# Kernel optimization log

Measured on AMD Instinct MI355X. Metric: run time of the kernel, lower is better.

The kernel has to match this reference:

```python
import jax, jax.numpy as jnp
import numpy as np
from functools import partial

NUM_HEADS = 12
RATIO_ACT = 0.5   # prune_ratio_act_store
RATIO_ATTN = 0.5  # prune_ratio_attn_mat_store


def kth_mask(x, ratio):
    # torch.kthvalue semantics: threshold = k-th SMALLEST of |x| over the flat tensor
    n = x.size
    k = int(np.clip(n * ratio, 1, n))
    mag = jnp.abs(x)
    thr = jnp.sort(mag.reshape(-1))[k - 1]
    return (mag >= thr).astype(x.dtype)


def st(dense, prune):
    # straight-through: value = dense, gradient flows through `prune` path
    return jax.lax.stop_gradient(dense) + prune - jax.lax.stop_gradient(prune)


def _softmax_prune_impl(x, ratio):
    dense = jax.nn.softmax(x, axis=-1)
    mask = kth_mask(dense, ratio)
    return dense, mask * dense


@partial(jax.custom_vjp, nondiff_argnums=(1,))
def softmax_prune(x, ratio):
    return _softmax_prune_impl(x, ratio)


def _sp_fwd(x, ratio):
    dense, sparse = _softmax_prune_impl(x, ratio)
    return (dense, sparse), sparse


def _sp_bwd(ratio, A, cots):
    # custom backward uses the SPARSE probs in the softmax Jacobian; the
    # cotangent of the sparse output is ignored (matches the torch Function)
    g_dense, _ = cots
    g = A * (g_dense - jnp.sum(g_dense * A, axis=-1, keepdims=True))
    return (g,)


softmax_prune.defvjp(_sp_fwd, _sp_bwd)


def setup_inputs() -> dict:
    key = jax.random.key(0)
    ks = jax.random.split(key, 5)
    B, S, H = 8, 577, 768
    hs = jax.random.normal(ks[0], (B, S, H), dtype=jnp.float32)
    w = lambda k: jax.random.normal(k, (H, H), dtype=jnp.float32) * 0.02
    z = jnp.zeros((H,), dtype=jnp.float32)
    return {
        "hidden_states": hs,
        "Wq": w(ks[1]), "bq": z,
        "Wk": w(ks[2]), "bk": z,
        "Wv": w(ks[3]), "bv": z,
        "Wo": w(ks[4]), "bo": z,
    }


def attention_forward(hidden_states, Wq, bq, Wk, bk, Wv, bv, Wo, bo):
    B, S, H = hidden_states.shape
    nh, hd = NUM_HEADS, H // NUM_HEADS
    sg = jax.lax.stop_gradient
    lin = lambda x, W, b: x @ W + b

    # prune hidden states by global magnitude threshold
    hs_p = sg(kth_mask(hidden_states, RATIO_ACT)) * hidden_states

    q = st(lin(hidden_states, Wq, bq), lin(hs_p, Wq, bq))
    k = st(lin(hidden_states, Wk, bk), lin(hs_p, Wk, bk))
    v = st(lin(hidden_states, Wv, bv), lin(hs_p, Wv, bv))

    heads = lambda x: x.reshape(B, S, nh, hd).transpose(0, 2, 1, 3)  # [B,h,S,d]
    q, k, v = heads(q), heads(k), heads(v)

    qp = sg(kth_mask(q, RATIO_ACT)) * q
    kp = sg(kth_mask(k, RATIO_ACT)) * k

    scores = st(jnp.einsum('bhqd,bhkd->bhqk', q, k),
                jnp.einsum('bhqd,bhkd->bhqk', qp, kp))
    scores = scores / float(np.sqrt(hd))

    probs, probs_p = softmax_prune(scores, RATIO_ATTN)  # dropout rate = 0 -> identity

    vp = sg(kth_mask(v, RATIO_ACT)) * v
    ctx = st(jnp.einsum('bhqk,bhkd->bhqd', probs, v),
             jnp.einsum('bhqk,bhkd->bhqd', probs_p, vp))

    ctx = ctx.transpose(0, 2, 1, 3).reshape(B, S, H)
    ctx_p = sg(kth_mask(ctx, RATIO_ACT)) * ctx

    out = st(lin(ctx, Wo, bo), lin(ctx_p, Wo, bo))
    return out  # vis=False -> weights is None


def reference(hidden_states, Wq, bq, Wk, bk, Wv, bv, Wo, bo):
    return attention_forward(hidden_states, Wq, bq, Wk, bk, Wv, bv, Wo, bo)
```

## Files before the change

### kernel.cpp

```cpp
#include <hip/hip_runtime.h>
#include <hip/hip_bf16.h>


#define B_ 8
#define S_ 577
#define H_ 768
#define NH_ 12
#define HD_ 64
#define M_ (B_*S_)
#define MPAD 4736
#define BH_ (B_*NH_)
#define SKPAD 640
#define LTS 136

typedef __attribute__((ext_vector_type(8))) short short8;
typedef __attribute__((ext_vector_type(4))) short s16x4;
typedef __attribute__((ext_vector_type(4))) float f32x4;

__device__ inline unsigned short f2bf(float f){
    unsigned int u = __float_as_uint(f);
    u = u + 0x7fffu + ((u>>16)&1u);
    return (unsigned short)(u>>16);
}

__device__ inline void gload_lds16(const short* g, short* l){
    __builtin_amdgcn_global_load_lds((const __attribute__((address_space(1))) void*)g,
                                     (__attribute__((address_space(3))) void*)l, 16, 0, 0);
}

__global__ __launch_bounds__(256) void k_prep(
    const float* __restrict__ hs, short* __restrict__ abf,
    const float* __restrict__ Wq, const float* __restrict__ Wk,
    const float* __restrict__ Wv, const float* __restrict__ Wo,
    short* __restrict__ Tq, short* __restrict__ Tk,
    short* __restrict__ Tv, short* __restrict__ To,
    short* __restrict__ kh, short* __restrict__ vt)
{
    const int bid = blockIdx.x, t = threadIdx.x;
    if(bid < 1776){
        int i = bid*256 + t;
        if(bid >= 1731){ *(short8*)(abf + (size_t)i*8) = (short8){}; return; }
        const float4* p = (const float4*)(hs + (size_t)i*8);
        float4 a = p[0], b = p[1];
        short8 v;
        v[0]=(short)f2bf(a.x); v[1]=(short)f2bf(a.y); v[2]=(short)f2bf(a.z); v[3]=(short)f2bf(a.w);
        v[4]=(short)f2bf(b.x); v[5]=(short)f2bf(b.y); v[6]=(short)f2bf(b.z); v[7]=(short)f2bf(b.w);
        *(short8*)(abf + (size_t)i*8) = v;
    } else if(bid < 2352){
        int zidx = bid - 1776;
        int z = zidx & 3, rem = zidx >> 2;
        int kx = rem % 12, ny = rem / 12;
        const float* W = z==0?Wq: z==1?Wk: z==2?Wv:Wo;
        short*       T = z==0?Tq: z==1?Tk: z==2?Tv:To;
        __shared__ float lds[64][65];
        int k0 = kx*64, n0 = ny*64;
        for(int i=0;i<4;i++){
            int row = i*16 + (t>>4);
            int col = (t&15)*4;
            float4 v = *(const float4*)&W[(k0+row)*768 + n0 + col];
            lds[row][col]=v.x; lds[row][col+1]=v.y; lds[row][col+2]=v.z; lds[row][col+3]=v.w;
        }
        __syncthreads();
        for(int i=0;i<4;i++){
            int n = i*16 + (t>>4);
            int k4 = (t&15)*4;
            for(int j=0;j<4;j++)
                T[(n0+n)*768 + k0 + k4 + j] = (short)f2bf(lds[k4+j][n]);
        }
    } else {
        int tid = (bid-2352)*256 + t;
        short8 z = {};
        if(tid < 48384){
            int row_id = tid>>3, ch = tid&7;
            int bh = row_id/63, r = row_id - bh*63;
            *(short8*)&kh[((size_t)bh*SKPAD + 577 + r)*64 + ch*8] = z;
        } else if(tid < 97536){
            int j = tid - 48384;
            int row_id = j>>3, ch = j&7;
            int bh = row_id>>6, d = row_id&63;
            *(short8*)&vt[((size_t)bh*64 + d)*SKPAD + 576 + ch*8] = z;
        }
    }
}

__global__ __launch_bounds__(512) void k_gemm(
    const short* __restrict__ A, const short* __restrict__ T,
    const float* __restrict__ b0, const float* __restrict__ b1, const float* __restrict__ b2,
    short* __restrict__ oq, short* __restrict__ ok, short* __restrict__ ovt,
    float* __restrict__ of, int mode, int NT)
{
    __shared__ short sh[32768];
    const int t = threadIdx.x;

    const int nwg = gridDim.x;
    const int q8 = nwg>>3, r8 = nwg&7;
    const int xcd = blockIdx.x&7, cidx = blockIdx.x>>3;
    const int wg = (xcd<r8 ? xcd*(q8+1) : r8*(q8+1) + (xcd-r8)*q8) + cidx;
    const int mt = wg/NT, ntile = wg - mt*NT;
    const int m0 = mt*128, n0 = ntile*128;

    const int seg = (mode==3)? 0 : n0/768;
    const float* bias = (mode==3)? b0 : (seg==0?b0: seg==1?b1:b2);
    const int nlb = (mode==3)? n0 : n0 - seg*768;

    const int w = t>>6, lane = t&63, g = lane>>4, c = lane&15;
    const int wm = w>>1, wn = w&1;

    const int lrow = lane>>3;
    const int lcol = ((lane&7) ^ lrow) * 8;
    const short* pa = A + (size_t)(m0 + w*8 + lrow)*768 + lcol;
    const short* pb = T + (size_t)(n0 + w*8 + lrow)*768 + lcol;

    f32x4 acc[2][4] = {};

    #pragma unroll
    for(int i=0;i<2;i++){
        gload_lds16(pa + (size_t)(i*64)*768, &sh[(i*64 + w*8)*64]);
        gload_lds16(pb + (size_t)(i*64)*768, &sh[8192 + (i*64 + w*8)*64]);
    }
    int bb = 0;
    for(int kk=0; kk<12; kk++){
        if(kk<11){
            short* dstA = &sh[(bb^1)*16384];
            short* dstB = dstA + 8192;
            #pragma unroll
            for(int i=0;i<2;i++){
                gload_lds16(pa + (size_t)(i*64)*768 + (kk+1)*64, &dstA[(i*64 + w*8)*64]);
                gload_lds16(pb + (size_t)(i*64)*768 + (kk+1)*64, &dstB[(i*64 + w*8)*64]);
            }
            asm volatile("s_waitcnt vmcnt(4)" ::: "memory");
        } else {
            asm volatile("s_waitcnt vmcnt(0)" ::: "memory");
        }
        __builtin_amdgcn_s_barrier();
        asm volatile("" ::: "memory");

        const short* LA = &sh[bb*16384];
        const short* LB = LA + 8192;
        short8 af[2][2], bfv[4][2];
        #pragma unroll
        for(int mi=0; mi<2; mi++){
            int row = wm*32 + mi*16 + c;
            int rx = (row&7)<<3;
            af[mi][0] = *(const short8*)&LA[row*64 + ((g*8) ^ rx)];
            af[mi][1] = *(const short8*)&LA[row*64 + ((32 + g*8) ^ rx)];
        }
        #pragma unroll
        for(int ni=0; ni<4; ni++){
            int row = wn*64 + ni*16 + c;
            int rx = (row&7)<<3;
            bfv[ni][0] = *(const short8*)&LB[row*64 + ((g*8) ^ rx)];
            bfv[ni][1] = *(const short8*)&LB[row*64 + ((32 + g*8) ^ rx)];
        }
        __builtin_amdgcn_s_setprio(1);
        #pragma unroll
        for(int mi=0; mi<2; mi++)
            #pragma unroll
            for(int ni=0; ni<4; ni++){
                acc[mi][ni] = __builtin_amdgcn_mfma_f32_16x16x32_bf16(af[mi][0], bfv[ni][0], acc[mi][ni], 0,0,0);
                acc[mi][ni] = __builtin_amdgcn_mfma_f32_16x16x32_bf16(af[mi][1], bfv[ni][1], acc[mi][ni], 0,0,0);
            }
        __builtin_amdgcn_s_setprio(0);
        asm volatile("s_waitcnt lgkmcnt(0)" ::: "memory");
        __builtin_amdgcn_s_barrier();
        asm volatile("" ::: "memory");
        bb ^= 1;
    }

    if(mode==3){
        #pragma unroll
        for(int mi=0; mi<2; mi++) for(int ni=0; ni<4; ni++){
            #pragma unroll
            for(int r=0; r<4; r++){
                int m = m0 + wm*32 + mi*16 + g*4 + r;
                int n = n0 + wn*64 + ni*16 + c;
                if(m >= M_) continue;
                of[(size_t)m*768 + n] = acc[mi][ni][r] + bias[n];
            }
        }
        return;
    }

    if(seg==2){
        #pragma unroll
        for(int mi=0;mi<2;mi++)
            #pragma unroll
            for(int ni=0;ni<4;ni++){
                int nl_ = wn*64 + ni*16 + c;
                float bv = bias[nlb + nl_];
                s16x4 pk;
                #pragma unroll
                for(int r=0;r<4;r++) pk[r] = (short)f2bf(acc[mi][ni][r] + bv);
                int ml0 = wm*32 + mi*16 + g*4;
                *(s16x4*)&sh[nl_*LTS + ml0] = pk;
            }
    } else {
        #pragma unroll
        for(int mi=0;mi<2;mi++)
            #pragma unroll
            for(int ni=0;ni<4;ni++){
                int nl_ = wn*64 + ni*16 + c;
                float bv = bias[nlb + nl_];
                #pragma unroll
                for(int r=0;r<4;r++){
                    int ml = wm*32 + mi*16 + g*4 + r;
                    sh[ml*LTS + nl_] = (short)f2bf(acc[mi][ni][r] + bv);
                }
            }
    }
    __syncthreads();

    #pragma unroll
    for(int i=0;i<4;i++){
        int idx = i*512 + t;
        int rp = idx>>4, ch = idx&15;
        short8 v8 = *(const short8*)&sh[rp*LTS + ch*8];
        if(seg==2){
            int nl = nlb + rp, hh = nl>>6, dd = nl&63;
            int mg = m0 + ch*8;
            if(mg < M_){
                int b0_ = mg/S_, s0 = mg - b0_*S_;
                if(s0+7 < S_ && mg+7 < M_){
                    *(short8*)&ovt[(((size_t)b0_*NH_+hh)*HD_+dd)*SKPAD + s0] = v8;
                } else {
                    for(int j=0;j<8;j++){
                        int m=mg+j;
                        if(m<M_){ int bj=m/S_, sj=m-bj*S_;
                            ovt[(((size_t)bj*NH_+hh)*HD_+dd)*SKPAD+sj]=v8[j]; }
                    }
                }
            }
        } else {
            int m = m0 + rp;
            if(m < M_){
                int b0_ = m/S_, s0 = m - b0_*S_;
                int nl = nlb + ch*8, hh = nl>>6, dd = nl&63;
                if(seg==1) *(short8*)&ok[(((size_t)b0_*NH_+hh)*SKPAD + s0)*HD_ + dd] = v8;
                else       *(short8*)&oq[(((size_t)b0_*NH_+hh)*S_   + s0)*HD_ + dd] = v8;
            }
        }
    }
}

__global__ __launch_bounds__(256) void k_attn(
    const short* __restrict__ qh, const short* __restrict__ kh, const short* __restrict__ vt,
    short* __restrict__ ctx)
{
    __shared__ short lK[2][64*64], lV[2][64*64], lP[4*2048];
    const int t = threadIdx.x;
    const int w = t>>6, lane = t&63, g = lane>>4, c = lane&15;
    const int bh = blockIdx.x, b = bh/NH_, h = bh%NH_;
    const int q0 = blockIdx.y*128;

    #pragma unroll
    for(int i=0;i<4;i++){
        int row = i*8 + (lane>>3);
        int e8 = (lane&7)*8;
        int s = q0 + w*32 + row;
        short8 v = {};
        if(s < S_) v = *(const short8*)&qh[((size_t)bh*S_ + s)*HD_ + e8];
        *(short8*)&lP[w*2048 + row*64 + (e8 ^ ((row&7)<<3))] = v;
    }
    short8 qf[2][2];
    #pragma unroll
    for(int qi=0; qi<2; qi++)
        #pragma unroll
        for(int ks=0; ks<2; ks++)
            qf[qi][ks] = *(const short8*)&lP[w*2048 + (qi*16+c)*64 + ((ks*32+g*8) ^ ((c&7)<<3))];

    short8 ones;
    #pragma unroll
    for(int j=0;j<8;j++) ones[j] = (short)0x3F80;

    const int srow = lane>>3;
    const int sw8 = ((lane&7) ^ srow)*8;
    const short* pk0 = kh + ((size_t)bh*SKPAD + w*16 + srow)*64 + sw8;
    const short* pv0 = vt + ((size_t)bh*64 + w*16 + srow)*SKPAD + sw8;

    #pragma unroll
    for(int i=0;i<2;i++){
        gload_lds16(pk0 + i*8*64,    &lK[0][(w*16+i*8)*64]);
        gload_lds16(pv0 + i*8*SKPAD, &lV[0][(w*16+i*8)*64]);
    }

    float m_run[2][4], l_run[2][4];
    f32x4 O[2][4] = {};
    #pragma unroll
    for(int qi=0;qi<2;qi++)
        #pragma unroll
        for(int r=0;r<4;r++){ m_run[qi][r] = -3e38f; l_run[qi][r] = 0.f; }

    int bb = 0;
    for(int kt=0; kt<10; kt++){
        if(kt<9){
            const short* pk = pk0 + (kt+1)*4096;
            const short* pv = pv0 + (kt+1)*64;
            #pragma unroll
            for(int i=0;i<2;i++){
                gload_lds16(pk + i*8*64,    &lK[bb^1][(w*16+i*8)*64]);
                gload_lds16(pv + i*8*SKPAD, &lV[bb^1][(w*16+i*8)*64]);
            }
            asm volatile("s_waitcnt vmcnt(4)" ::: "memory");
        } else {
            asm volatile("s_waitcnt vmcnt(0)" ::: "memory");
        }
        __builtin_amdgcn_s_barrier();
        asm volatile("" ::: "memory");

        const short* LK = lK[bb]; const short* LV = lV[bb];

        float sv[2][4][4];
        #pragma unroll
        for(int nt=0; nt<4; nt++){
            int row = nt*16 + c;
            int rx = (row&7)<<3;
            short8 kf[2];
            kf[0] = *(const short8*)&LK[row*64 + ((g*8) ^ rx)];
            kf[1] = *(const short8*)&LK[row*64 + ((32+g*8) ^ rx)];
            __builtin_amdgcn_s_setprio(1);
            #pragma unroll
            for(int qi=0; qi<2; qi++){
                f32x4 sa = {};
                sa = __builtin_amdgcn_mfma_f32_16x16x32_bf16(qf[qi][0], kf[0], sa, 0,0,0);
                sa = __builtin_amdgcn_mfma_f32_16x16x32_bf16(qf[qi][1], kf[1], sa, 0,0,0);
                #pragma unroll
                for(int r=0;r<4;r++) sv[qi][nt][r] = sa[r]*0.18033688011f;
            }
            __builtin_amdgcn_s_setprio(0);
        }
        if(kt==9){
            #pragma unroll
            for(int nt=0; nt<4; nt++){
                int key = 576 + nt*16 + c;
                if(key >= S_){
                    #pragma unroll
                    for(int qi=0;qi<2;qi++)
                        #pragma unroll
                        for(int r=0;r<4;r++) sv[qi][nt][r] = -3e38f;
                }
            }
        }
        float fac[2][4];
        #pragma unroll
        for(int qi=0; qi<2; qi++)
            #pragma unroll
            for(int r=0;r<4;r++){
                float mx = fmaxf(fmaxf(sv[qi][0][r],sv[qi][1][r]),fmaxf(sv[qi][2][r],sv[qi][3][r]));
                for(int off=1; off<16; off<<=1) mx = fmaxf(mx, __shfl_xor(mx, off));
                float nm = fmaxf(m_run[qi][r], mx);
                fac[qi][r] = __builtin_amdgcn_exp2f(m_run[qi][r] - nm);
                m_run[qi][r] = nm;
            }
        #pragma unroll
        for(int qi=0; qi<2; qi++)
            #pragma unroll
            for(int nt=0; nt<4; nt++)
                #pragma unroll
                for(int r=0;r<4;r++){
                    float p = __builtin_amdgcn_exp2f(sv[qi][nt][r] - m_run[qi][r]);
                    int prow = g*4 + r;
                    lP[w*2048 + qi*1024 + prow*64 + ((nt*16 + c) ^ ((prow&7)<<3))] = (short)f2bf(p);
                }
        short8 pf[2][2];
        #pragma unroll
        for(int qi=0; qi<2; qi++)
            #pragma unroll
            for(int ks=0; ks<2; ks++)
                pf[qi][ks] = *(const short8*)&lP[w*2048 + qi*1024 + c*64 + ((ks*32+g*8) ^ ((c&7)<<3))];
        __builtin_amdgcn_s_setprio(1);
        #pragma unroll
        for(int qi=0; qi<2; qi++){
            f32x4 rs = {};
            rs = __builtin_amdgcn_mfma_f32_16x16x32_bf16(pf[qi][0], ones, rs, 0,0,0);
            rs = __builtin_amdgcn_mfma_f32_16x16x32_bf16(pf[qi][1], ones, rs, 0,0,0);
            #pragma unroll
            for(int r=0;r<4;r++) l_run[qi][r] = l_run[qi][r]*fac[qi][r] + rs[r];
        }
        __builtin_amdgcn_s_setprio(0);
        #pragma unroll
        for(int qi=0; qi<2; qi++)
            #pragma unroll
            for(int nt=0;nt<4;nt++)
                #pragma unroll
                for(int r=0;r<4;r++) O[qi][nt][r] *= fac[qi][r];

        __builtin_amdgcn_s_setprio(1);
        #pragma unroll
        for(int nt=0; nt<4; nt++){
            int vrow = nt*16 + c;
            int rx = (vrow&7)<<3;
            short8 vf[2];
            vf[0] = *(const short8*)&LV[vrow*64 + ((g*8) ^ rx)];
            vf[1] = *(const short8*)&LV[vrow*64 + ((32+g*8) ^ rx)];
            #pragma unroll
            for(int qi=0; qi<2; qi++){
                O[qi][nt] = __builtin_amdgcn_mfma_f32_16x16x32_bf16(pf[qi][0], vf[0], O[qi][nt], 0,0,0);
                O[qi][nt] = __builtin_amdgcn_mfma_f32_16x16x32_bf16(pf[qi][1], vf[1], O[qi][nt], 0,0,0);
            }
        }
        __builtin_amdgcn_s_setprio(0);
        asm volatile("s_waitcnt lgkmcnt(0)" ::: "memory");
        __builtin_amdgcn_s_barrier();
        asm volatile("" ::: "memory");
        bb ^= 1;
    }

    #pragma unroll
    for(int qi=0; qi<2; qi++)
        #pragma unroll
        for(int nt=0; nt<4; nt++)
            #pragma unroll
            for(int r=0;r<4;r++){
                int s = q0 + w*32 + qi*16 + g*4 + r;
                if(s < S_){
                    float val = O[qi][nt][r] / l_run[qi][r];
                    ctx[((size_t)b*S_ + s)*H_ + h*HD_ + nt*16 + c] = (short)f2bf(val);
                }
            }
}

extern "C" void kernel_launch(void* const* d_in, const int* in_sizes, int n_in,
                              void* d_out, int out_size, void* d_ws, size_t ws_size,
                              hipStream_t stream)
{
    const float* hs = (const float*)d_in[0];
    const float* Wq = (const float*)d_in[1];
    const float* bq = (const float*)d_in[2];
    const float* Wk = (const float*)d_in[3];
    const float* bk = (const float*)d_in[4];
    const float* Wv = (const float*)d_in[5];
    const float* bv = (const float*)d_in[6];
    const float* Wo = (const float*)d_in[7];
    const float* bo = (const float*)d_in[8];
    float* out = (float*)d_out;

    char* ws = (char*)d_ws;
    short* abf = (short*)(ws);
    short* ctx = abf;
    short* wqt = (short*)(ws + 7274496);
    short* wkt = (short*)(ws + 7274496 + 1179648);
    short* wvt = (short*)(ws + 7274496 + 2*1179648);
    short* wot = (short*)(ws + 7274496 + 3*1179648);
    short* qh  = (short*)(ws + 11993088);
    short* kh  = (short*)(ws + 19083264);
    short* vt  = (short*)(ws + 26947584);

    k_prep<<<2733, 256, 0, stream>>>(hs, abf, Wq,Wk,Wv,Wo, wqt,wkt,wvt,wot, kh, vt);
    k_gemm<<<666, 512, 0, stream>>>(abf, wqt, bq,bk,bv, qh,kh,vt, nullptr, 0, 18);
    k_attn<<<dim3(96,5), 256, 0, stream>>>(qh, kh, vt, ctx);
    k_gemm<<<222, 512, 0, stream>>>(ctx, wot, bo,bo,bo, nullptr,nullptr,nullptr, out, 3, 6);
}
```

Measured before the change: 90.36 us.

## Use dedicated 256x256-tile QKV GEMM kernel with staged double-buffered LDS

Moves the QKV projection out of the generic GEMM into a new kernel with 256x256 tiles, 128 KB of double-buffered LDS and a phased MFMA schedule that prefetches the next k-tile while computing. The epilogue is split into two passes that write the Q/K/V head layouts. Larger tiles raise operand reuse and cut the number of tile loads, but the grid drops from 666 to 171 workgroups on a 256-CU part, which leaves many CUs idle. The output-projection GEMM is simplified to a single fp32-output mode.

```diff
diff --git a/kernel.cpp b/kernel.cpp
--- a/kernel.cpp
+++ b/kernel.cpp
@@ -12,6 +12,7 @@
 #define BH_ (B_*NH_)
 #define SKPAD 640
 #define LTS 136
+#define LTS2 264
 
 typedef __attribute__((ext_vector_type(8))) short short8;
 typedef __attribute__((ext_vector_type(4))) short s16x4;
@@ -83,11 +84,223 @@
     }
 }
 
+__global__ __launch_bounds__(512) void k_qkv(
+    const short* __restrict__ A, const short* __restrict__ T,
+    const float* __restrict__ b0, const float* __restrict__ b1, const float* __restrict__ b2,
+    short* __restrict__ oq, short* __restrict__ ok, short* __restrict__ ovt)
+{
+    __shared__ short sh[65536];
+    const int t = threadIdx.x;
+
+    const int nwg = gridDim.x;
+    const int q8 = nwg>>3, r8 = nwg&7;
+    const int xcd = blockIdx.x&7, cidx = blockIdx.x>>3;
+    const int wg = (xcd<r8 ? xcd*(q8+1) : r8*(q8+1) + (xcd-r8)*q8) + cidx;
+    const int mt = wg/9, nt9 = wg - mt*9;
+    const int m0 = mt*256, n0 = nt9*256;
+    const int seg = n0/768;
+    const float* bias = (seg==0?b0: seg==1?b1:b2);
+    const int nlb = n0 - seg*768;
+
+    const int w = t>>6, lane = t&63, g = lane>>4, c = lane&15;
+    const int wm = w>>2, wn = w&3;
+
+    const int srow = t>>3, sch = t&7;
+    const int sx = (sch ^ (srow&7))*8;
+    const short* pa[2][2]; const short* pb[2][2];
+    #pragma unroll
+    for(int hf=0; hf<2; hf++)
+        #pragma unroll
+        for(int i=0;i<2;i++){
+            int rga = m0 + hf*128 + i*64 + srow;
+            if(rga > 4735) rga = 4735;
+            pa[hf][i] = A + (size_t)rga*768 + sx;
+            pb[hf][i] = T + (size_t)(n0 + hf*128 + i*64 + srow)*768 + sx;
+        }
+    const int dof = srow*64 + sch*8;
+
+    f32x4 acc[8][4] = {};
+
+    #define STAGE(tt) { int pS = ((tt)&1)*16384; int kof = (tt)*64;              \
+        _Pragma("unroll") for(int hf=0; hf<2; hf++){                             \
+            _Pragma("unroll") for(int i=0;i<2;i++){                              \
+                gload_lds16(pa[hf][i] + kof, &sh[pS + hf*8192 + i*4096 + dof]);  \
+                gload_lds16(pb[hf][i] + kof, &sh[32768 + pS + hf*8192 + i*4096 + dof]); } } }
+
+    STAGE(0);
+    asm volatile("s_waitcnt vmcnt(0)" ::: "memory");
+    __builtin_amdgcn_s_barrier();
+    asm volatile("" ::: "memory");
+
+    for(int kt=0; kt<12; kt++){
+        const int p = (kt&1)*16384;
+        const short* LA = &sh[p + wm*8192];
+        const short* LB = &sh[32768 + p + (wn>>1)*8192];
+        const int brow0 = (wn&1)*64;
+
+        short8 af[4][2], af2[4][2], bfv[4][2];
+        #pragma unroll
+        for(int mi=0; mi<4; mi++){
+            int rih = mi*16 + c, rx = (rih&7)<<3;
+            af[mi][0] = *(const short8*)&LA[rih*64 + ((g*8) ^ rx)];
+            af[mi][1] = *(const short8*)&LA[rih*64 + ((32+g*8) ^ rx)];
+        }
+        #pragma unroll
+        for(int ni=0; ni<2; ni++){
+            int rih = brow0 + ni*16 + c, rx = (rih&7)<<3;
+            bfv[ni][0] = *(const short8*)&LB[rih*64 + ((g*8) ^ rx)];
+            bfv[ni][1] = *(const short8*)&LB[rih*64 + ((32+g*8) ^ rx)];
+        }
+        if(kt < 11) STAGE(kt+1);
+        __builtin_amdgcn_s_barrier();
+        asm volatile("s_waitcnt lgkmcnt(0)" ::: "memory");
+        __builtin_amdgcn_s_setprio(1);
+        #pragma unroll
+        for(int mi=0; mi<4; mi++)
+            #pragma unroll
+            for(int ni=0; ni<2; ni++){
+                acc[mi][ni] = __builtin_amdgcn_mfma_f32_16x16x32_bf16(af[mi][0], bfv[ni][0], acc[mi][ni], 0,0,0);
+                acc[mi][ni] = __builtin_amdgcn_mfma_f32_16x16x32_bf16(af[mi][1], bfv[ni][1], acc[mi][ni], 0,0,0);
+            }
+        __builtin_amdgcn_s_setprio(0);
+        __builtin_amdgcn_s_barrier();
+        asm volatile("" ::: "memory");
+
+        #pragma unroll
+        for(int ni=2; ni<4; ni++){
+            int rih = brow0 + ni*16 + c, rx = (rih&7)<<3;
+            bfv[ni][0] = *(const short8*)&LB[rih*64 + ((g*8) ^ rx)];
+            bfv[ni][1] = *(const short8*)&LB[rih*64 + ((32+g*8) ^ rx)];
+        }
+        __builtin_amdgcn_s_barrier();
+        asm volatile("s_waitcnt lgkmcnt(0)" ::: "memory");
+        __builtin_amdgcn_s_setprio(1);
+        #pragma unroll
+        for(int mi=0; mi<4; mi++)
+            #pragma unroll
+            for(int ni=2; ni<4; ni++){
+                acc[mi][ni] = __builtin_amdgcn_mfma_f32_16x16x32_bf16(af[mi][0], bfv[ni][0], acc[mi][ni], 0,0,0);
+                acc[mi][ni] = __builtin_amdgcn_mfma_f32_16x16x32_bf16(af[mi][1], bfv[ni][1], acc[mi][ni], 0,0,0);
+            }
+        __builtin_amdgcn_s_setprio(0);
+        __builtin_amdgcn_s_barrier();
+        asm volatile("" ::: "memory");
+
+        #pragma unroll
+        for(int mi=0; mi<4; mi++){
+            int rih = 64 + mi*16 + c, rx = (rih&7)<<3;
+            af2[mi][0] = *(const short8*)&LA[rih*64 + ((g*8) ^ rx)];
+            af2[mi][1] = *(const short8*)&LA[rih*64 + ((32+g*8) ^ rx)];
+        }
+        __builtin_amdgcn_s_barrier();
+        asm volatile("s_waitcnt lgkmcnt(0)" ::: "memory");
+        __builtin_amdgcn_s_setprio(1);
+        #pragma unroll
+        for(int mi=0; mi<4; mi++)
+            #pragma unroll
+            for(int ni=0; ni<2; ni++){
+                acc[4+mi][ni] = __builtin_amdgcn_mfma_f32_16x16x32_bf16(af2[mi][0], bfv[ni][0], acc[4+mi][ni], 0,0,0);
+                acc[4+mi][ni] = __builtin_amdgcn_mfma_f32_16x16x32_bf16(af2[mi][1], bfv[ni][1], acc[4+mi][ni], 0,0,0);
+            }
+        __builtin_amdgcn_s_setprio(0);
+        __builtin_amdgcn_s_barrier();
+        asm volatile("" ::: "memory");
+
+        __builtin_amdgcn_s_setprio(1);
+        #pragma unroll
+        for(int mi=0; mi<4; mi++)
+            #pragma unroll
+            for(int ni=2; ni<4; ni++){
+                acc[4+mi][ni] = __builtin_amdgcn_mfma_f32_16x16x32_bf16(af2[mi][0], bfv[ni][0], acc[4+mi][ni], 0,0,0);
+                acc[4+mi][ni] = __builtin_amdgcn_mfma_f32_16x16x32_bf16(af2[mi][1], bfv[ni][1], acc[4+mi][ni], 0,0,0);
+            }
+        __builtin_amdgcn_s_setprio(0);
+        asm volatile("s_waitcnt vmcnt(0)" ::: "memory");
+        __builtin_amdgcn_s_barrier();
+        asm volatile("" ::: "memory");
+    }
+    #undef STAGE
+
+    if(seg==2){
+        #pragma unroll
+        for(int cch=0; cch<2; cch++){
+            if((wn>>1) == cch){
+                #pragma unroll
+                for(int mi=0; mi<8; mi++)
+                    #pragma unroll
+                    for(int ni=0; ni<4; ni++){
+                        int nc = (wn&1)*64 + ni*16 + c;
+                        float bv = bias[nlb + cch*128 + nc];
+                        s16x4 pk;
+                        #pragma unroll
+                        for(int r=0;r<4;r++) pk[r] = (short)f2bf(acc[mi][ni][r] + bv);
+                        int ml0 = wm*128 + mi*16 + g*4;
+                        *(s16x4*)&sh[nc*LTS2 + ml0] = pk;
+                    }
+            }
+            __syncthreads();
+            #pragma unroll
+            for(int i=0;i<8;i++){
+                int idx = i*512 + t;
+                int rp = idx>>5, ch = idx&31;
+                short8 v8 = *(const short8*)&sh[rp*LTS2 + ch*8];
+                int nl = nlb + cch*128 + rp, hh = nl>>6, dd = nl&63;
+                int mg = m0 + ch*8;
+                if(mg < M_){
+                    int bb = mg/S_, s0 = mg - bb*S_;
+                    if(s0+7 < S_ && mg+7 < M_){
+                        *(short8*)&ovt[(((size_t)bb*NH_+hh)*HD_+dd)*SKPAD + s0] = v8;
+                    } else {
+                        for(int j=0;j<8;j++){
+                            int m=mg+j;
+                            if(m<M_){ int bj=m/S_, sj=m-bj*S_;
+                                ovt[(((size_t)bj*NH_+hh)*HD_+dd)*SKPAD+sj]=v8[j]; }
+                        }
+                    }
+                }
+            }
+            __syncthreads();
+        }
+    } else {
+        #pragma unroll
+        for(int cch=0; cch<2; cch++){
+            if(wm == cch){
+                #pragma unroll
+                for(int mi=0; mi<8; mi++)
+                    #pragma unroll
+                    for(int ni=0; ni<4; ni++){
+                        int nl_ = wn*64 + ni*16 + c;
+                        float bv = bias[nlb + nl_];
+                        #pragma unroll
+                        for(int r=0;r<4;r++){
+                            int ml = mi*16 + g*4 + r;
+                            sh[ml*LTS2 + nl_] = (short)f2bf(acc[mi][ni][r] + bv);
+                        }
+                    }
+            }
+            __syncthreads();
+            #pragma unroll
+            for(int i=0;i<8;i++){
+                int idx = i*512 + t;
+                int rp = idx>>5, ch = idx&31;
+                short8 v8 = *(const short8*)&sh[rp*LTS2 + ch*8];
+                int m = m0 + cch*128 + rp;
+                if(m < M_){
+                    int bb = m/S_, ss = m - bb*S_;
+                    int nl = nlb + ch*8, hh = nl>>6, dd = nl&63;
+                    if(seg==1) *(short8*)&ok[(((size_t)bb*NH_+hh)*SKPAD + ss)*HD_ + dd] = v8;
+                    else       *(short8*)&oq[(((size_t)bb*NH_+hh)*S_   + ss)*HD_ + dd] = v8;
+                }
+            }
+            __syncthreads();
+        }
+    }
+}
+
 __global__ __launch_bounds__(512) void k_gemm(
     const short* __restrict__ A, const short* __restrict__ T,
-    const float* __restrict__ b0, const float* __restrict__ b1, const float* __restrict__ b2,
-    short* __restrict__ oq, short* __restrict__ ok, short* __restrict__ ovt,
-    float* __restrict__ of, int mode, int NT)
+    const float* __restrict__ b0,
+    float* __restrict__ of, int NT)
 {
     __shared__ short sh[32768];
     const int t = threadIdx.x;
@@ -98,10 +311,7 @@
     const int wg = (xcd<r8 ? xcd*(q8+1) : r8*(q8+1) + (xcd-r8)*q8) + cidx;
     const int mt = wg/NT, ntile = wg - mt*NT;
     const int m0 = mt*128, n0 = ntile*128;
-
-    const int seg = (mode==3)? 0 : n0/768;
-    const float* bias = (mode==3)? b0 : (seg==0?b0: seg==1?b1:b2);
-    const int nlb = (mode==3)? n0 : n0 - seg*768;
+    const float* bias = b0;
 
     const int w = t>>6, lane = t&63, g = lane>>4, c = lane&15;
     const int wm = w>>1, wn = w&1;
@@ -167,77 +377,14 @@
         bb ^= 1;
     }
 
-    if(mode==3){
-        #pragma unroll
-        for(int mi=0; mi<2; mi++) for(int ni=0; ni<4; ni++){
-            #pragma unroll
-            for(int r=0; r<4; r++){
-                int m = m0 + wm*32 + mi*16 + g*4 + r;
-                int n = n0 + wn*64 + ni*16 + c;
-                if(m >= M_) continue;
-                of[(size_t)m*768 + n] = acc[mi][ni][r] + bias[n];
-            }
-        }
-        return;
-    }
-
-    if(seg==2){
-        #pragma unroll
-        for(int mi=0;mi<2;mi++)
-            #pragma unroll
-            for(int ni=0;ni<4;ni++){
-                int nl_ = wn*64 + ni*16 + c;
-                float bv = bias[nlb + nl_];
-                s16x4 pk;
-                #pragma unroll
-                for(int r=0;r<4;r++) pk[r] = (short)f2bf(acc[mi][ni][r] + bv);
-                int ml0 = wm*32 + mi*16 + g*4;
-                *(s16x4*)&sh[nl_*LTS + ml0] = pk;
-            }
-    } else {
-        #pragma unroll
-        for(int mi=0;mi<2;mi++)
-            #pragma unroll
-            for(int ni=0;ni<4;ni++){
-                int nl_ = wn*64 + ni*16 + c;
-                float bv = bias[nlb + nl_];
-                #pragma unroll
-                for(int r=0;r<4;r++){
-                    int ml = wm*32 + mi*16 + g*4 + r;
-                    sh[ml*LTS + nl_] = (short)f2bf(acc[mi][ni][r] + bv);
-                }
-            }
-    }
-    __syncthreads();
-
-    #pragma unroll
-    for(int i=0;i<4;i++){
-        int idx = i*512 + t;
-        int rp = idx>>4, ch = idx&15;
-        short8 v8 = *(const short8*)&sh[rp*LTS + ch*8];
-        if(seg==2){
-            int nl = nlb + rp, hh = nl>>6, dd = nl&63;
-            int mg = m0 + ch*8;
-            if(mg < M_){
-                int b0_ = mg/S_, s0 = mg - b0_*S_;
-                if(s0+7 < S_ && mg+7 < M_){
-                    *(short8*)&ovt[(((size_t)b0_*NH_+hh)*HD_+dd)*SKPAD + s0] = v8;
-                } else {
-                    for(int j=0;j<8;j++){
-                        int m=mg+j;
-                        if(m<M_){ int bj=m/S_, sj=m-bj*S_;
-                            ovt[(((size_t)bj*NH_+hh)*HD_+dd)*SKPAD+sj]=v8[j]; }
-                    }
-                }
-            }
-        } else {
-            int m = m0 + rp;
-            if(m < M_){
-                int b0_ = m/S_, s0 = m - b0_*S_;
-                int nl = nlb + ch*8, hh = nl>>6, dd = nl&63;
-                if(seg==1) *(short8*)&ok[(((size_t)b0_*NH_+hh)*SKPAD + s0)*HD_ + dd] = v8;
-                else       *(short8*)&oq[(((size_t)b0_*NH_+hh)*S_   + s0)*HD_ + dd] = v8;
-            }
+    #pragma unroll
+    for(int mi=0; mi<2; mi++) for(int ni=0; ni<4; ni++){
+        #pragma unroll
+        for(int r=0; r<4; r++){
+            int m = m0 + wm*32 + mi*16 + g*4 + r;
+            int n = n0 + wn*64 + ni*16 + c;
+            if(m >= M_) continue;
+            of[(size_t)m*768 + n] = acc[mi][ni][r] + bias[n];
         }
     }
 }
@@ -446,7 +593,7 @@
     short* vt  = (short*)(ws + 26947584);
 
     k_prep<<<2733, 256, 0, stream>>>(hs, abf, Wq,Wk,Wv,Wo, wqt,wkt,wvt,wot, kh, vt);
-    k_gemm<<<666, 512, 0, stream>>>(abf, wqt, bq,bk,bv, qh,kh,vt, nullptr, 0, 18);
+    k_qkv<<<171, 512, 0, stream>>>(abf, wqt, bq,bk,bv, qh,kh,vt);
     k_attn<<<dim3(96,5), 256, 0, stream>>>(qh, kh, vt, ctx);
-    k_gemm<<<222, 512, 0, stream>>>(ctx, wot, bo,bo,bo, nullptr,nullptr,nullptr, out, 3, 6);
-}
+    k_gemm<<<222, 512, 0, stream>>>(ctx, wot, bo, out, 6);
+}
```

Measured after the change: 97.67 us. 8.1% more time.

## Pre-block operands in MFMA fragment layout and load GEMM tiles directly to registers

Applied to the files above, without the earlier changes.

The prep kernel now writes activations and weights in a blocked layout that matches the 16x32 MFMA fragment order. The QKV and output-projection GEMMs are rewritten so each wave computes its own 64x64 tile, loading fragments straight from global memory into registers with double buffering instead of staging through LDS with barriers. This removes LDS traffic and block-wide synchronisation in the main loop. In exchange it gives up cross-wave operand reuse, which raises global and L2 load volume.

```diff
diff --git a/kernel.cpp b/kernel.cpp
--- a/kernel.cpp
+++ b/kernel.cpp
@@ -11,7 +11,7 @@
 #define MPAD 4736
 #define BH_ (B_*NH_)
 #define SKPAD 640
-#define LTS 136
+#define KT_ 24
 
 typedef __attribute__((ext_vector_type(8))) short short8;
 typedef __attribute__((ext_vector_type(4))) short s16x4;
@@ -29,29 +29,30 @@
 }
 
 __global__ __launch_bounds__(256) void k_prep(
-    const float* __restrict__ hs, short* __restrict__ abf,
+    const float* __restrict__ hs, short* __restrict__ ablk,
     const float* __restrict__ Wq, const float* __restrict__ Wk,
     const float* __restrict__ Wv, const float* __restrict__ Wo,
-    short* __restrict__ Tq, short* __restrict__ Tk,
-    short* __restrict__ Tv, short* __restrict__ To,
+    short* __restrict__ wblk, short* __restrict__ oblk,
     short* __restrict__ kh, short* __restrict__ vt)
 {
     const int bid = blockIdx.x, t = threadIdx.x;
     if(bid < 1776){
         int i = bid*256 + t;
-        if(bid >= 1731){ *(short8*)(abf + (size_t)i*8) = (short8){}; return; }
+        int row = i/96, k8 = i - row*96;
+        size_t dst = ((size_t)((row>>4)*KT_ + (k8>>2))*64 + (k8&3)*16 + (row&15))*8;
+        if(bid >= 1731){ *(short8*)(ablk + dst) = (short8){}; return; }
         const float4* p = (const float4*)(hs + (size_t)i*8);
         float4 a = p[0], b = p[1];
         short8 v;
         v[0]=(short)f2bf(a.x); v[1]=(short)f2bf(a.y); v[2]=(short)f2bf(a.z); v[3]=(short)f2bf(a.w);
         v[4]=(short)f2bf(b.x); v[5]=(short)f2bf(b.y); v[6]=(short)f2bf(b.z); v[7]=(short)f2bf(b.w);
-        *(short8*)(abf + (size_t)i*8) = v;
+        *(short8*)(ablk + dst) = v;
     } else if(bid < 2352){
         int zidx = bid - 1776;
         int z = zidx & 3, rem = zidx >> 2;
         int kx = rem % 12, ny = rem / 12;
         const float* W = z==0?Wq: z==1?Wk: z==2?Wv:Wo;
-        short*       T = z==0?Tq: z==1?Tk: z==2?Tv:To;
+        short* Dst = (z<3)? wblk : oblk;
         __shared__ float lds[64][65];
         int k0 = kx*64, n0 = ny*64;
         for(int i=0;i<4;i++){
@@ -61,11 +62,16 @@
             lds[row][col]=v.x; lds[row][col+1]=v.y; lds[row][col+2]=v.z; lds[row][col+3]=v.w;
         }
         __syncthreads();
-        for(int i=0;i<4;i++){
-            int n = i*16 + (t>>4);
-            int k4 = (t&15)*4;
-            for(int j=0;j<4;j++)
-                T[(n0+n)*768 + k0 + k4 + j] = (short)f2bf(lds[k4+j][n]);
+        #pragma unroll
+        for(int rep=0; rep<2; rep++){
+            int n_loc = (t>>3) + rep*32;
+            int k8 = t&7;
+            short8 v;
+            #pragma unroll
+            for(int j=0;j<8;j++) v[j] = (short)f2bf(lds[k8*8+j][n_loc]);
+            int nf = (z<3 ? z*768 : 0) + n0 + n_loc;
+            size_t dst = ((size_t)((nf>>4)*KT_ + (k0>>5) + (k8>>2))*64 + (k8&3)*16 + (nf&15))*8;
+            *(short8*)(Dst + dst) = v;
         }
     } else {
         int tid = (bid-2352)*256 + t;
@@ -83,163 +89,169 @@
     }
 }
 
-__global__ __launch_bounds__(512) void k_gemm(
-    const short* __restrict__ A, const short* __restrict__ T,
+__global__ __launch_bounds__(256,3) void k_qkv(
+    const short* __restrict__ ablk, const short* __restrict__ wblk,
     const float* __restrict__ b0, const float* __restrict__ b1, const float* __restrict__ b2,
-    short* __restrict__ oq, short* __restrict__ ok, short* __restrict__ ovt,
-    float* __restrict__ of, int mode, int NT)
+    short* __restrict__ oq, short* __restrict__ ok, short* __restrict__ ovt)
 {
-    __shared__ short sh[32768];
+    __shared__ short sh[4*64*72];
     const int t = threadIdx.x;
+    const int w = t>>6, lane = t&63, g = lane>>4, c = lane&15;
 
     const int nwg = gridDim.x;
     const int q8 = nwg>>3, r8 = nwg&7;
     const int xcd = blockIdx.x&7, cidx = blockIdx.x>>3;
     const int wg = (xcd<r8 ? xcd*(q8+1) : r8*(q8+1) + (xcd-r8)*q8) + cidx;
-    const int mt = wg/NT, ntile = wg - mt*NT;
-    const int m0 = mt*128, n0 = ntile*128;
-
-    const int seg = (mode==3)? 0 : n0/768;
-    const float* bias = (mode==3)? b0 : (seg==0?b0: seg==1?b1:b2);
-    const int nlb = (mode==3)? n0 : n0 - seg*768;
-
-    const int w = t>>6, lane = t&63, g = lane>>4, c = lane&15;
-    const int wm = w>>1, wn = w&1;
-
-    const int lrow = lane>>3;
-    const int lcol = ((lane&7) ^ lrow) * 8;
-    const short* pa = A + (size_t)(m0 + w*8 + lrow)*768 + lcol;
-    const short* pb = T + (size_t)(n0 + w*8 + lrow)*768 + lcol;
-
-    f32x4 acc[2][4] = {};
-
-    #pragma unroll
-    for(int i=0;i<2;i++){
-        gload_lds16(pa + (size_t)(i*64)*768, &sh[(i*64 + w*8)*64]);
-        gload_lds16(pb + (size_t)(i*64)*768, &sh[8192 + (i*64 + w*8)*64]);
-    }
-    int bb = 0;
-    for(int kk=0; kk<12; kk++){
-        if(kk<11){
-            short* dstA = &sh[(bb^1)*16384];
-            short* dstB = dstA + 8192;
-            #pragma unroll
-            for(int i=0;i<2;i++){
-                gload_lds16(pa + (size_t)(i*64)*768 + (kk+1)*64, &dstA[(i*64 + w*8)*64]);
-                gload_lds16(pb + (size_t)(i*64)*768 + (kk+1)*64, &dstB[(i*64 + w*8)*64]);
-            }
-            asm volatile("s_waitcnt vmcnt(4)" ::: "memory");
-        } else {
-            asm volatile("s_waitcnt vmcnt(0)" ::: "memory");
-        }
-        __builtin_amdgcn_s_barrier();
-        asm volatile("" ::: "memory");
-
-        const short* LA = &sh[bb*16384];
-        const short* LB = LA + 8192;
-        short8 af[2][2], bfv[4][2];
-        #pragma unroll
-        for(int mi=0; mi<2; mi++){
-            int row = wm*32 + mi*16 + c;
-            int rx = (row&7)<<3;
-            af[mi][0] = *(const short8*)&LA[row*64 + ((g*8) ^ rx)];
-            af[mi][1] = *(const short8*)&LA[row*64 + ((32 + g*8) ^ rx)];
-        }
-        #pragma unroll
-        for(int ni=0; ni<4; ni++){
-            int row = wn*64 + ni*16 + c;
-            int rx = (row&7)<<3;
-            bfv[ni][0] = *(const short8*)&LB[row*64 + ((g*8) ^ rx)];
-            bfv[ni][1] = *(const short8*)&LB[row*64 + ((32 + g*8) ^ rx)];
-        }
-        __builtin_amdgcn_s_setprio(1);
-        #pragma unroll
-        for(int mi=0; mi<2; mi++)
-            #pragma unroll
-            for(int ni=0; ni<4; ni++){
-                acc[mi][ni] = __builtin_amdgcn_mfma_f32_16x16x32_bf16(af[mi][0], bfv[ni][0], acc[mi][ni], 0,0,0);
-                acc[mi][ni] = __builtin_amdgcn_mfma_f32_16x16x32_bf16(af[mi][1], bfv[ni][1], acc[mi][ni], 0,0,0);
-            }
-        __builtin_amdgcn_s_setprio(0);
-        asm volatile("s_waitcnt lgkmcnt(0)" ::: "memory");
-        __builtin_amdgcn_s_barrier();
-        asm volatile("" ::: "memory");
-        bb ^= 1;
-    }
-
-    if(mode==3){
-        #pragma unroll
-        for(int mi=0; mi<2; mi++) for(int ni=0; ni<4; ni++){
-            #pragma unroll
-            for(int r=0; r<4; r++){
-                int m = m0 + wm*32 + mi*16 + g*4 + r;
-                int n = n0 + wn*64 + ni*16 + c;
-                if(m >= M_) continue;
-                of[(size_t)m*768 + n] = acc[mi][ni][r] + bias[n];
-            }
-        }
-        return;
-    }
-
+    const int gw = wg*4 + w;
+    const int mtile = gw/36, ntile = gw - mtile*36;
+    const int seg = ntile/12;
+    const int nl64 = (ntile - seg*12)*64;
+    const float* bias = (seg==0?b0: seg==1?b1:b2);
+
+    const short* pa = ablk + ((size_t)(mtile*4)*KT_)*512 + lane*8;
+    const short* pw = wblk + ((size_t)(ntile*4)*KT_)*512 + lane*8;
+
+    f32x4 acc[4][4] = {};
+    short8 a0[4], bf0[4], a1[4], bf1[4];
+
+    #define LD(AA,BB,kt) { _Pragma("unroll") for(int x=0;x<4;x++){            \
+        AA[x] = *(const short8*)(pa + ((size_t)x*KT_ + (kt))*512);            \
+        BB[x] = *(const short8*)(pw + ((size_t)x*KT_ + (kt))*512); } }
+    #define FM(AA,BB) { _Pragma("unroll") for(int mi=0;mi<4;mi++)             \
+        _Pragma("unroll") for(int ni=0;ni<4;ni++)                             \
+        acc[mi][ni] = __builtin_amdgcn_mfma_f32_16x16x32_bf16(AA[mi], BB[ni], acc[mi][ni],0,0,0); }
+
+    LD(a0,bf0,0);
+    #pragma unroll 1
+    for(int it=0; it<11; it++){
+        LD(a1,bf1, 2*it+1);
+        FM(a0,bf0);
+        LD(a0,bf0, 2*it+2);
+        FM(a1,bf1);
+    }
+    LD(a1,bf1, 23);
+    FM(a0,bf0);
+    FM(a1,bf1);
+    #undef LD
+    #undef FM
+
+    short* my = sh + w*4608;
+    const int h = nl64>>6;
+    const int m0 = mtile*64;
     if(seg==2){
         #pragma unroll
-        for(int mi=0;mi<2;mi++)
+        for(int mi=0;mi<4;mi++)
             #pragma unroll
             for(int ni=0;ni<4;ni++){
-                int nl_ = wn*64 + ni*16 + c;
-                float bv = bias[nlb + nl_];
+                int nl_ = ni*16 + c;
+                float bv = bias[nl64 + nl_];
                 s16x4 pk;
                 #pragma unroll
                 for(int r=0;r<4;r++) pk[r] = (short)f2bf(acc[mi][ni][r] + bv);
-                int ml0 = wm*32 + mi*16 + g*4;
-                *(s16x4*)&sh[nl_*LTS + ml0] = pk;
+                *(s16x4*)&my[nl_*72 + mi*16 + g*4] = pk;
             }
     } else {
         #pragma unroll
-        for(int mi=0;mi<2;mi++)
+        for(int mi=0;mi<4;mi++)
             #pragma unroll
             for(int ni=0;ni<4;ni++){
-                int nl_ = wn*64 + ni*16 + c;
-                float bv = bias[nlb + nl_];
+                int nl_ = ni*16 + c;
+                float bv = bias[nl64 + nl_];
                 #pragma unroll
-                for(int r=0;r<4;r++){
-                    int ml = wm*32 + mi*16 + g*4 + r;
-                    sh[ml*LTS + nl_] = (short)f2bf(acc[mi][ni][r] + bv);
-                }
-            }
-    }
-    __syncthreads();
-
-    #pragma unroll
-    for(int i=0;i<4;i++){
-        int idx = i*512 + t;
-        int rp = idx>>4, ch = idx&15;
-        short8 v8 = *(const short8*)&sh[rp*LTS + ch*8];
-        if(seg==2){
-            int nl = nlb + rp, hh = nl>>6, dd = nl&63;
-            int mg = m0 + ch*8;
+                for(int r=0;r<4;r++)
+                    my[(mi*16+g*4+r)*72 + nl_] = (short)f2bf(acc[mi][ni][r] + bv);
+            }
+    }
+    asm volatile("s_waitcnt lgkmcnt(0)" ::: "memory");
+
+    const int lr8 = lane>>3, lch = lane&7;
+    if(seg==2){
+        #pragma unroll
+        for(int j=0;j<8;j++){
+            int d = j*8 + lr8;
+            short8 v8 = *(const short8*)&my[d*72 + lch*8];
+            int mg = m0 + lch*8;
             if(mg < M_){
-                int b0_ = mg/S_, s0 = mg - b0_*S_;
+                int bb = mg/S_, s0 = mg - bb*S_;
                 if(s0+7 < S_ && mg+7 < M_){
-                    *(short8*)&ovt[(((size_t)b0_*NH_+hh)*HD_+dd)*SKPAD + s0] = v8;
+                    *(short8*)&ovt[(((size_t)bb*NH_+h)*HD_+d)*SKPAD + s0] = v8;
                 } else {
-                    for(int j=0;j<8;j++){
-                        int m=mg+j;
+                    for(int jj=0;jj<8;jj++){
+                        int m=mg+jj;
                         if(m<M_){ int bj=m/S_, sj=m-bj*S_;
-                            ovt[(((size_t)bj*NH_+hh)*HD_+dd)*SKPAD+sj]=v8[j]; }
+                            ovt[(((size_t)bj*NH_+h)*HD_+d)*SKPAD+sj]=v8[jj]; }
                     }
                 }
             }
-        } else {
-            int m = m0 + rp;
+        }
+    } else {
+        #pragma unroll
+        for(int j=0;j<8;j++){
+            int m = m0 + j*8 + lr8;
             if(m < M_){
-                int b0_ = m/S_, s0 = m - b0_*S_;
-                int nl = nlb + ch*8, hh = nl>>6, dd = nl&63;
-                if(seg==1) *(short8*)&ok[(((size_t)b0_*NH_+hh)*SKPAD + s0)*HD_ + dd] = v8;
-                else       *(short8*)&oq[(((size_t)b0_*NH_+hh)*S_   + s0)*HD_ + dd] = v8;
-            }
-        }
-    }
+                short8 v8 = *(const short8*)&my[(j*8+lr8)*72 + lch*8];
+                int bb = m/S_, ss = m - bb*S_;
+                if(seg==1) *(short8*)&ok[(((size_t)bb*NH_+h)*SKPAD + ss)*HD_ + lch*8] = v8;
+                else       *(short8*)&oq[(((size_t)bb*NH_+h)*S_   + ss)*HD_ + lch*8] = v8;
+            }
+        }
+    }
+}
+
+__global__ __launch_bounds__(256,3) void k_oproj(
+    const short* __restrict__ ctx, const short* __restrict__ oblk,
+    const float* __restrict__ bo, float* __restrict__ of)
+{
+    const int t = threadIdx.x;
+    const int w = t>>6, lane = t&63, g = lane>>4, c = lane&15;
+
+    const int nwg = gridDim.x;
+    const int q8 = nwg>>3, r8 = nwg&7;
+    const int xcd = blockIdx.x&7, cidx = blockIdx.x>>3;
+    const int wg = (xcd<r8 ? xcd*(q8+1) : r8*(q8+1) + (xcd-r8)*q8) + cidx;
+    const int gw = wg*4 + w;
+    const int mtile = gw/12, ntile = gw - mtile*12;
+    const int m0 = mtile*64, n0 = ntile*64;
+
+    const short* pa = ctx + (size_t)(m0 + c)*768 + g*8;
+    const short* pw = oblk + ((size_t)(ntile*4)*KT_)*512 + lane*8;
+
+    f32x4 acc[4][4] = {};
+    short8 a0[4], bf0[4], a1[4], bf1[4];
+
+    #define LD(AA,BB,kt) { _Pragma("unroll") for(int x=0;x<4;x++){            \
+        AA[x] = *(const short8*)(pa + (size_t)x*16*768 + (kt)*32);            \
+        BB[x] = *(const short8*)(pw + ((size_t)x*KT_ + (kt))*512); } }
+    #define FM(AA,BB) { _Pragma("unroll") for(int mi=0;mi<4;mi++)             \
+        _Pragma("unroll") for(int ni=0;ni<4;ni++)                             \
+        acc[mi][ni] = __builtin_amdgcn_mfma_f32_16x16x32_bf16(AA[mi], BB[ni], acc[mi][ni],0,0,0); }
+
+    LD(a0,bf0,0);
+    #pragma unroll 1
+    for(int it=0; it<11; it++){
+        LD(a1,bf1, 2*it+1);
+        FM(a0,bf0);
+        LD(a0,bf0, 2*it+2);
+        FM(a1,bf1);
+    }
+    LD(a1,bf1, 23);
+    FM(a0,bf0);
+    FM(a1,bf1);
+    #undef LD
+    #undef FM
+
+    #pragma unroll
+    for(int mi=0; mi<4; mi++)
+        #pragma unroll
+        for(int ni=0; ni<4; ni++){
+            #pragma unroll
+            for(int r=0; r<4; r++){
+                int m = m0 + mi*16 + g*4 + r;
+                int n = n0 + ni*16 + c;
+                if(m >= M_) continue;
+                of[(size_t)m*768 + n] = acc[mi][ni][r] + bo[n];
+            }
+        }
 }
 
 __global__ __launch_bounds__(256) void k_attn(
@@ -435,18 +447,16 @@
     float* out = (float*)d_out;
 
     char* ws = (char*)d_ws;
-    short* abf = (short*)(ws);
-    short* ctx = abf;
-    short* wqt = (short*)(ws + 7274496);
-    short* wkt = (short*)(ws + 7274496 + 1179648);
-    short* wvt = (short*)(ws + 7274496 + 2*1179648);
-    short* wot = (short*)(ws + 7274496 + 3*1179648);
-    short* qh  = (short*)(ws + 11993088);
-    short* kh  = (short*)(ws + 19083264);
-    short* vt  = (short*)(ws + 26947584);
-
-    k_prep<<<2733, 256, 0, stream>>>(hs, abf, Wq,Wk,Wv,Wo, wqt,wkt,wvt,wot, kh, vt);
-    k_gemm<<<666, 512, 0, stream>>>(abf, wqt, bq,bk,bv, qh,kh,vt, nullptr, 0, 18);
+    short* ablk = (short*)(ws);
+    short* ctx  = ablk;
+    short* wblk = (short*)(ws + 7274496);
+    short* oblk = (short*)(ws + 10813440);
+    short* qh   = (short*)(ws + 11993088);
+    short* kh   = (short*)(ws + 19083264);
+    short* vt   = (short*)(ws + 26947584);
+
+    k_prep<<<2733, 256, 0, stream>>>(hs, ablk, Wq,Wk,Wv,Wo, wblk, oblk, kh, vt);
+    k_qkv<<<666, 256, 0, stream>>>(ablk, wblk, bq,bk,bv, qh,kh,vt);
     k_attn<<<dim3(96,5), 256, 0, stream>>>(qh, kh, vt, ctx);
-    k_gemm<<<222, 512, 0, stream>>>(ctx, wot, bo,bo,bo, nullptr,nullptr,nullptr, out, 3, 6);
-}
+    k_oproj<<<222, 256, 0, stream>>>(ctx, oblk, bo, out);
+}
```

Result: slower. 102.3 us (+13.2%).

## Load K/V fragments directly from global memory instead of LDS double-buffering

Applied to the files above, without the earlier changes.

The attention kernel drops its shared-memory double-buffered K and V tiles and the per-tile barriers. Each wave now reads its own K and V MFMA fragments straight from global memory into registers every key tile. This removes LDS traffic and block synchronisation, but every wave now reads the full K/V itself (4x redundant global/L2 reads), and there is no software prefetch to hide the load latency.

```diff
diff --git a/kernel.cpp b/kernel.cpp
--- a/kernel.cpp
+++ b/kernel.cpp
@@ -246,7 +246,7 @@
     const short* __restrict__ qh, const short* __restrict__ kh, const short* __restrict__ vt,
     short* __restrict__ ctx)
 {
-    __shared__ short lK[2][64*64], lV[2][64*64], lP[4*2048];
+    __shared__ short lP[4*2048];
     const int t = threadIdx.x;
     const int w = t>>6, lane = t&63, g = lane>>4, c = lane&15;
     const int bh = blockIdx.x, b = bh/NH_, h = bh%NH_;
@@ -272,16 +272,8 @@
     #pragma unroll
     for(int j=0;j<8;j++) ones[j] = (short)0x3F80;
 
-    const int srow = lane>>3;
-    const int sw8 = ((lane&7) ^ srow)*8;
-    const short* pk0 = kh + ((size_t)bh*SKPAD + w*16 + srow)*64 + sw8;
-    const short* pv0 = vt + ((size_t)bh*64 + w*16 + srow)*SKPAD + sw8;
-
-    #pragma unroll
-    for(int i=0;i<2;i++){
-        gload_lds16(pk0 + i*8*64,    &lK[0][(w*16+i*8)*64]);
-        gload_lds16(pv0 + i*8*SKPAD, &lV[0][(w*16+i*8)*64]);
-    }
+    const short* Kb = kh + (size_t)bh*SKPAD*64 + (size_t)c*64 + g*8;
+    const short* Vb = vt + (size_t)bh*64*SKPAD + (size_t)c*SKPAD + g*8;
 
     float m_run[2][4], l_run[2][4];
     f32x4 O[2][4] = {};
@@ -290,39 +282,29 @@
         #pragma unroll
         for(int r=0;r<4;r++){ m_run[qi][r] = -3e38f; l_run[qi][r] = 0.f; }
 
-    int bb = 0;
+    #pragma unroll 1
     for(int kt=0; kt<10; kt++){
-        if(kt<9){
-            const short* pk = pk0 + (kt+1)*4096;
-            const short* pv = pv0 + (kt+1)*64;
-            #pragma unroll
-            for(int i=0;i<2;i++){
-                gload_lds16(pk + i*8*64,    &lK[bb^1][(w*16+i*8)*64]);
-                gload_lds16(pv + i*8*SKPAD, &lV[bb^1][(w*16+i*8)*64]);
-            }
-            asm volatile("s_waitcnt vmcnt(4)" ::: "memory");
-        } else {
-            asm volatile("s_waitcnt vmcnt(0)" ::: "memory");
-        }
-        __builtin_amdgcn_s_barrier();
-        asm volatile("" ::: "memory");
-
-        const short* LK = lK[bb]; const short* LV = lV[bb];
+        const int key0 = kt*64;
+        short8 kf[4][2], vf[4][2];
+        #pragma unroll
+        for(int nt=0; nt<4; nt++){
+            const short* kr = Kb + (size_t)(key0 + nt*16)*64;
+            kf[nt][0] = *(const short8*)(kr);
+            kf[nt][1] = *(const short8*)(kr + 32);
+            const short* vr = Vb + (size_t)(nt*16)*SKPAD + key0;
+            vf[nt][0] = *(const short8*)(vr);
+            vf[nt][1] = *(const short8*)(vr + 32);
+        }
 
         float sv[2][4][4];
         #pragma unroll
         for(int nt=0; nt<4; nt++){
-            int row = nt*16 + c;
-            int rx = (row&7)<<3;
-            short8 kf[2];
-            kf[0] = *(const short8*)&LK[row*64 + ((g*8) ^ rx)];
-            kf[1] = *(const short8*)&LK[row*64 + ((32+g*8) ^ rx)];
             __builtin_amdgcn_s_setprio(1);
             #pragma unroll
             for(int qi=0; qi<2; qi++){
                 f32x4 sa = {};
-                sa = __builtin_amdgcn_mfma_f32_16x16x32_bf16(qf[qi][0], kf[0], sa, 0,0,0);
-                sa = __builtin_amdgcn_mfma_f32_16x16x32_bf16(qf[qi][1], kf[1], sa, 0,0,0);
+                sa = __builtin_amdgcn_mfma_f32_16x16x32_bf16(qf[qi][0], kf[nt][0], sa, 0,0,0);
+                sa = __builtin_amdgcn_mfma_f32_16x16x32_bf16(qf[qi][1], kf[nt][1], sa, 0,0,0);
                 #pragma unroll
                 for(int r=0;r<4;r++) sv[qi][nt][r] = sa[r]*0.18033688011f;
             }
@@ -386,23 +368,13 @@
 
         __builtin_amdgcn_s_setprio(1);
         #pragma unroll
-        for(int nt=0; nt<4; nt++){
-            int vrow = nt*16 + c;
-            int rx = (vrow&7)<<3;
-            short8 vf[2];
-            vf[0] = *(const short8*)&LV[vrow*64 + ((g*8) ^ rx)];
-            vf[1] = *(const short8*)&LV[vrow*64 + ((32+g*8) ^ rx)];
+        for(int nt=0; nt<4; nt++)
             #pragma unroll
             for(int qi=0; qi<2; qi++){
-                O[qi][nt] = __builtin_amdgcn_mfma_f32_16x16x32_bf16(pf[qi][0], vf[0], O[qi][nt], 0,0,0);
-                O[qi][nt] = __builtin_amdgcn_mfma_f32_16x16x32_bf16(pf[qi][1], vf[1], O[qi][nt], 0,0,0);
-            }
-        }
+                O[qi][nt] = __builtin_amdgcn_mfma_f32_16x16x32_bf16(pf[qi][0], vf[nt][0], O[qi][nt], 0,0,0);
+                O[qi][nt] = __builtin_amdgcn_mfma_f32_16x16x32_bf16(pf[qi][1], vf[nt][1], O[qi][nt], 0,0,0);
+            }
         __builtin_amdgcn_s_setprio(0);
-        asm volatile("s_waitcnt lgkmcnt(0)" ::: "memory");
-        __builtin_amdgcn_s_barrier();
-        asm volatile("" ::: "memory");
-        bb ^= 1;
     }
 
     #pragma unroll
```

Result: slower. 102.3 us (+13.2%).
